# Kernel optimization log

Hardware: AMD Instinct MI355X
Metric: run time of the kernel (lower is better)

Reference implementation:

```python
import jax, jax.numpy as jnp
import numpy as np

BN, T, D_MODEL = 128, 256, 128
D_INNER, D_STATE, D_CONV, DT_RANK = 2 * D_MODEL, 16, 4, 8  # mamba-ssm defaults


def silu(v):
    return v * jax.nn.sigmoid(v)


def setup_inputs() -> dict:
    key = jax.random.key(0)
    ks = jax.random.split(key, 8)
    s = 0.02
    A_log = jnp.log(jnp.tile(jnp.arange(1, D_STATE + 1, dtype=jnp.float32), (D_INNER, 1)))
    return {
        "x": jax.random.normal(ks[0], (BN, T, D_MODEL), jnp.float32),
        "in_proj_w": jax.random.normal(ks[1], (2 * D_INNER, D_MODEL), jnp.float32) * s,
        "conv_w": jax.random.normal(ks[2], (D_INNER, 1, D_CONV), jnp.float32) * s,
        "conv_b": jnp.zeros((D_INNER,), jnp.float32),
        "x_proj_w": jax.random.normal(ks[3], (DT_RANK + 2 * D_STATE, D_INNER), jnp.float32) * s,
        "dt_proj_w": jax.random.normal(ks[4], (D_INNER, DT_RANK), jnp.float32) * s,
        "dt_proj_b": jax.random.uniform(ks[5], (D_INNER,), jnp.float32, -4.0, -2.0),
        "A_log": A_log,
        "D": jnp.ones((D_INNER,), jnp.float32),
        "out_proj_w": jax.random.normal(ks[6], (D_MODEL, D_INNER), jnp.float32) * s,
        "down_w": jax.random.normal(ks[7], (D_MODEL, D_MODEL, 3), jnp.float32) * s,
        "down_b": jnp.zeros((D_MODEL,), jnp.float32),
        "ln_g": jnp.ones((D_MODEL,), jnp.float32),
        "ln_b": jnp.zeros((D_MODEL,), jnp.float32),
    }


def _mamba(x, in_proj_w, conv_w, conv_b, x_proj_w, dt_proj_w, dt_proj_b, A_log, D, out_proj_w):
    B = x.shape[0]
    xz = jnp.einsum('bld,ed->ble', x, in_proj_w)            # (B,L,2*di)
    xc, z = jnp.split(xz, 2, axis=-1)
    # depthwise causal conv over time
    xt = xc.transpose(0, 2, 1)                               # (B,di,L)
    xt = jax.lax.conv_general_dilated(xt, conv_w, (1,), [(D_CONV - 1, 0)],
                                      feature_group_count=D_INNER)
    xc = silu((xt + conv_b[None, :, None]).transpose(0, 2, 1))  # (B,L,di)
    x_dbl = jnp.einsum('bld,ed->ble', xc, x_proj_w)
    dt, Bm, Cm = jnp.split(x_dbl, [DT_RANK, DT_RANK + D_STATE], axis=-1)
    delta = jax.nn.softplus(jnp.einsum('blr,dr->bld', dt, dt_proj_w) + dt_proj_b)  # (B,L,di)
    A = -jnp.exp(A_log)                                       # (di,N)

    def step(h, inp):
        d_t, B_t, C_t, u_t = inp                              # (B,di),(B,N),(B,N),(B,di)
        dA = jnp.exp(d_t[..., None] * A)                      # (B,di,N)
        h = dA * h + (d_t * u_t)[..., None] * B_t[:, None, :]
        return h, jnp.einsum('bdn,bn->bd', h, C_t)

    h0 = jnp.zeros((B, D_INNER, D_STATE), x.dtype)
    _, ys = jax.lax.scan(step, h0, (delta.swapaxes(0, 1), Bm.swapaxes(0, 1),
                                    Cm.swapaxes(0, 1), xc.swapaxes(0, 1)))
    y = ys.swapaxes(0, 1) + xc * D                            # (B,L,di)
    y = y * silu(z)
    return jnp.einsum('ble,de->bld', y, out_proj_w)


def reference(x, in_proj_w, conv_w, conv_b, x_proj_w, dt_proj_w, dt_proj_b,
              A_log, D, out_proj_w, down_w, down_b, ln_g, ln_b):
    x_skip = x
    h = _mamba(x, in_proj_w, conv_w, conv_b, x_proj_w, dt_proj_w, dt_proj_b,
               A_log, D, out_proj_w)                          # dropout: eval mode = identity
    ht = h.transpose(0, 2, 1)                                 # (B,d,T)
    ht = jax.lax.conv_general_dilated(ht, down_w, (2,), [(1, 1)]) + down_b[None, :, None]
    h = ht.transpose(0, 2, 1)                                 # (B,T//2,d)
    mu = jnp.mean(h, axis=-1, keepdims=True)
    var = jnp.mean((h - mu) ** 2, axis=-1, keepdims=True)
    h = (h - mu) * jax.lax.rsqrt(var + 1e-5) * ln_g + ln_b
    return (h, x_skip)
```

## Files before the change

### kernel.cpp

```cpp
#include <hip/hip_runtime.h>
#include <hip/hip_bf16.h>


typedef __attribute__((ext_vector_type(8))) short bf16x8;
typedef __attribute__((ext_vector_type(4))) short bf16x4;
typedef __attribute__((ext_vector_type(4))) float f32x4;
using bf16 = __hip_bfloat16;

static __device__ __forceinline__ short f2s(float v) {
  union { bf16 b; short s; } u; u.b = (bf16)v; return u.s;
}
static __device__ __forceinline__ float s2f(short s) {
  union { short s; bf16 b; } u; u.s = s; return (float)u.b;
}

static __device__ __forceinline__ size_t pidx(int b, int d, int t) {
  return ((((size_t)b * 8 + (d >> 5)) * 32 + (t >> 3)) * 32 + (d & 31)) * 8 + (t & 7);
}

__global__ __launch_bounds__(256) void prep_all(const float* __restrict__ x,
                                                const float* __restrict__ ipw,
                                                const float* __restrict__ xpw,
                                                const float* __restrict__ dwn,
                                                const float* __restrict__ opw,
                                                short* __restrict__ xb,
                                                float* __restrict__ out1,
                                                short* __restrict__ ipwb,
                                                short* __restrict__ wxb,
                                                short* __restrict__ G) {
  const int bid = blockIdx.x;
  if (bid < 4096) {
    int i = (bid * 256 + threadIdx.x) * 4;
    f32x4 v = *(const f32x4*)(x + i);
    bf16x4 o;
    o[0] = f2s(v[0]); o[1] = f2s(v[1]); o[2] = f2s(v[2]); o[3] = f2s(v[3]);
    *(bf16x4*)(xb + i) = o;
    *(f32x4*)(out1 + i) = v;
  } else if (bid < 4416) {
    int idx = (bid - 4096) * 256 + threadIdx.x;
    if (idx < 65536) {
      ipwb[idx] = f2s(ipw[idx]);
    } else {
      int j = idx - 65536;
      int n = j >> 8;
      wxb[j] = (n < 40) ? f2s(xpw[j]) : (short)0;
    }
  } else {
    const int jb = bid - 4416;
    const int k  = jb >> 7;
    const int co = jb & 127;
    const int e  = threadIdx.x;
    float acc = 0.f;
    for (int dm = 0; dm < 128; ++dm) {
      acc += dwn[(co * 128 + dm) * 3 + k] * opw[dm * 256 + e];
    }
    G[(size_t)(k * 128 + co) * 256 + e] = f2s(acc);
  }
}

__global__ __launch_bounds__(256, 2) void front_k(const short* __restrict__ xb,
                                                  const short* __restrict__ ipwb,
                                                  const short* __restrict__ wxb,
                                                  const float* __restrict__ cw,
                                                  const float* __restrict__ cb,
                                                  const float* __restrict__ dtw,
                                                  const float* __restrict__ dtb,
                                                  short* __restrict__ xcP,
                                                  short* __restrict__ dP,
                                                  short* __restrict__ zP,
                                                  float* __restrict__ SBC) {
  const int b  = blockIdx.x >> 2;
  const int t0 = (blockIdx.x & 3) * 64;
  const int w    = threadIdx.x >> 6;
  const int lane = threadIdx.x & 63;
  const int r16  = lane & 15;
  const int quad = lane >> 4;
  __shared__ short AL[80][136];
  __shared__ short XC[80][264];
  __shared__ short LT[64][72];
  __shared__ float DTL[64][8];
  for (int c = threadIdx.x; c < 1280; c += 256) {
    const int row = c >> 4;
    const int col = (c & 15) * 8;
    const int t = t0 - 16 + row;
    bf16x8 v = {};
    if (t >= 0) v = *(const bf16x8*)(xb + ((size_t)(b * 256 + t)) * 128 + col);
    *(bf16x8*)(&AL[row][col]) = v;
  }
  __syncthreads();
  {
    f32x4 acc[5][4] = {};
#pragma unroll
    for (int ks = 0; ks < 4; ++ks) {
      const int k0 = ks * 32;
      bf16x8 wf[4];
#pragma unroll
      for (int j = 0; j < 4; ++j)
        wf[j] = *(const bf16x8*)(ipwb +
                 (size_t)(w * 64 + j * 16 + r16) * 128 + quad * 8 + k0);
#pragma unroll
      for (int mt = 0; mt < 5; ++mt) {
        bf16x8 a = *(const bf16x8*)(&AL[mt * 16 + r16][quad * 8 + k0]);
#pragma unroll
        for (int j = 0; j < 4; ++j)
          acc[mt][j] = __builtin_amdgcn_mfma_f32_16x16x32_bf16(a, wf[j],
                                                               acc[mt][j], 0, 0, 0);
      }
    }
#pragma unroll
    for (int mt = 0; mt < 5; ++mt)
#pragma unroll
      for (int j = 0; j < 4; ++j)
#pragma unroll
        for (int r = 0; r < 4; ++r)
          XC[mt * 16 + quad * 4 + r][w * 64 + j * 16 + r16] = f2s(acc[mt][j][r]);
  }
  for (int nt = 0; nt < 4; ++nt) {
    f32x4 accz[4] = {};
#pragma unroll
    for (int ks = 0; ks < 4; ++ks) {
      const int k0 = ks * 32;
      bf16x8 a = *(const bf16x8*)(&AL[16 + w * 16 + r16][quad * 8 + k0]);
#pragma unroll
      for (int j = 0; j < 4; ++j) {
        bf16x8 wf = *(const bf16x8*)(ipwb +
                 (size_t)(256 + nt * 64 + j * 16 + r16) * 128 + quad * 8 + k0);
        accz[j] = __builtin_amdgcn_mfma_f32_16x16x32_bf16(a, wf, accz[j], 0, 0, 0);
      }
    }
    __syncthreads();
#pragma unroll
    for (int j = 0; j < 4; ++j)
#pragma unroll
      for (int r = 0; r < 4; ++r) {
        float v = accz[j][r];
        LT[j * 16 + r16][w * 16 + quad * 4 + r] = f2s(v / (1.f + __expf(-v)));
      }
    __syncthreads();
#pragma unroll
    for (int it = 0; it < 2; ++it) {
      const int dw = (threadIdx.x >> 3) + it * 32;
      const int tc = (threadIdx.x & 7) * 8;
      bf16x8 v = *(const bf16x8*)(&LT[dw][tc]);
      *(bf16x8*)(zP + pidx(b, nt * 64 + dw, t0 + tc)) = v;
    }
  }
  __syncthreads();
  bf16x8 cv[4][2];
#pragma unroll
  for (int dt_ = 0; dt_ < 4; ++dt_) {
    const int d = dt_ * 64 + lane;
    const float w0 = cw[d * 4], w1 = cw[d * 4 + 1];
    const float w2 = cw[d * 4 + 2], w3 = cw[d * 4 + 3];
    const float bias = cb[d];
    const int rb_ = 16 + w * 16;
    float p0 = s2f(XC[rb_ - 3][d]);
    float p1 = s2f(XC[rb_ - 2][d]);
    float p2 = s2f(XC[rb_ - 1][d]);
#pragma unroll
    for (int i = 0; i < 16; ++i) {
      const float cur = s2f(XC[rb_ + i][d]);
      const float a = bias + p0 * w0 + p1 * w1 + p2 * w2 + cur * w3;
      const short s = f2s(a / (1.f + __expf(-a)));
      cv[dt_][i >> 3][i & 7] = s;
      p0 = p1; p1 = p2; p2 = cur;
    }
    *(bf16x8*)(xcP + pidx(b, d, t0 + w * 16))     = cv[dt_][0];
    *(bf16x8*)(xcP + pidx(b, d, t0 + w * 16 + 8)) = cv[dt_][1];
  }
  __syncthreads();
#pragma unroll
  for (int dt_ = 0; dt_ < 4; ++dt_) {
    const int d = dt_ * 64 + lane;
#pragma unroll
    for (int i = 0; i < 16; ++i)
      XC[16 + w * 16 + i][d] = cv[dt_][i >> 3][i & 7];
  }
  __syncthreads();
  {
    f32x4 ax[4] = {};
#pragma unroll
    for (int ks = 0; ks < 8; ++ks) {
      const int k0 = ks * 32;
      bf16x8 a = *(const bf16x8*)(&XC[16 + w * 16 + r16][quad * 8 + k0]);
#pragma unroll
      for (int j = 0; j < 4; ++j) {
        bf16x8 wf = *(const bf16x8*)(wxb + (size_t)(j * 16 + r16) * 256 + quad * 8 + k0);
        ax[j] = __builtin_amdgcn_mfma_f32_16x16x32_bf16(a, wf, ax[j], 0, 0, 0);
      }
    }
#pragma unroll
    for (int j = 0; j < 4; ++j) {
      const int col = j * 16 + r16;
#pragma unroll
      for (int r = 0; r < 4; ++r) {
        const int tl = w * 16 + quad * 4 + r;
        if (col < 8) {
          DTL[tl][col] = ax[j][r];
        } else if (col < 40) {
          SBC[((size_t)b * 256 + t0 + tl) * 32 + (col - 8)] = ax[j][r];
        }
      }
    }
  }
  __syncthreads();
#pragma unroll
  for (int dt_ = 0; dt_ < 4; ++dt_) {
    const int d = dt_ * 64 + lane;
    float wd[8];
#pragma unroll
    for (int j = 0; j < 8; ++j) wd[j] = dtw[d * 8 + j];
    const float bd = dtb[d];
    bf16x8 dv0, dv1;
#pragma unroll
    for (int i = 0; i < 16; ++i) {
      const int tl = w * 16 + i;
      const f32x4 p0 = *(const f32x4*)(&DTL[tl][0]);
      const f32x4 p1 = *(const f32x4*)(&DTL[tl][4]);
      float acc = bd;
#pragma unroll
      for (int j = 0; j < 4; ++j) acc += p0[j] * wd[j] + p1[j] * wd[4 + j];
      const float delta = (acc > 20.f) ? acc : __logf(1.f + __expf(acc));
      const short s = f2s(delta);
      if (i < 8) dv0[i] = s; else dv1[i - 8] = s;
    }
    *(bf16x8*)(dP + pidx(b, d, t0 + w * 16))     = dv0;
    *(bf16x8*)(dP + pidx(b, d, t0 + w * 16 + 8)) = dv1;
  }
}

#define LDS_S(SB, CH) do {                                                   \
    _Pragma("unroll")                                                        \
    for (int j_ = 0; j_ < 8; ++j_) {                                         \
      SBr[SB][j_] = *(const f32x4*)(&S[(CH) * 8 + j_][q * 4]);               \
      SCr[SB][j_] = *(const f32x4*)(&S[(CH) * 8 + j_][16 + q * 4]);          \
    }                                                                        \
  } while (0)

#define LDG(GB, CH) do {                                                     \
    if ((CH) < 32) {                                                         \
      uu[GB] = *(const bf16x8*)(xcP + pb + (size_t)(CH) * 256);              \
      dd[GB] = *(const bf16x8*)(dP + pb + (size_t)(CH) * 256);               \
      if (q == 0) zz[GB] = *(const bf16x8*)(zP + pb + (size_t)(CH) * 256);   \
    }                                                                        \
  } while (0)

#define CHUNK(GB, SB, CH) do {                                               \
    _Pragma("unroll")                                                        \
    for (int tt_ = 0; tt_ < 8; ++tt_) {                                      \
      const int t_ = (CH) * 8 + tt_;                                         \
      const float delta_ = s2f(dd[GB][tt_]);                                 \
      const float u_ = s2f(uu[GB][tt_]);                                     \
      const float du_ = delta_ * u_;                                         \
      const f32x4 Bq_ = SBr[SB][tt_];                                        \
      const f32x4 Cq_ = SCr[SB][tt_];                                        \
      float yt_ = 0.f;                                                       \
      _Pragma("unroll")                                                      \
      for (int n_ = 0; n_ < 4; ++n_) {                                       \
        const float dA_ = __builtin_amdgcn_exp2f(delta_ * A2[n_]);           \
        h[n_] = dA_ * h[n_] + du_ * Bq_[n_];                                 \
        yt_ += h[n_] * Cq_[n_];                                              \
      }                                                                      \
      yt_ += __shfl_xor(yt_, 1);                                             \
      yt_ += __shfl_xor(yt_, 2);                                             \
      if (q == 0)                                                            \
        yb[(rb + t_) * 256 + d] = f2s((yt_ + u_ * Dv) * s2f(zz[GB][tt_]));   \
    }                                                                        \
  } while (0)

__global__ __launch_bounds__(128, 2) void scan12(const float* __restrict__ SBC,
                                                 const short* __restrict__ xcP,
                                                 const short* __restrict__ dP,
                                                 const short* __restrict__ zP,
                                                 const float* __restrict__ alog,
                                                 const float* __restrict__ Dp,
                                                 short* __restrict__ yb) {
  const int g = blockIdx.x & 7;
  const int b = blockIdx.x >> 3;
  const int q = threadIdx.x & 3;
  const int dl = threadIdx.x >> 2;
  const int d = g * 32 + dl;
  const size_t rb = (size_t)b * 256;
  __shared__ float S[256][32];
  for (int i = threadIdx.x; i < 2048; i += 128) {
    *(f32x4*)(&S[i >> 3][(i & 7) * 4]) =
        *(const f32x4*)(SBC + (size_t)b * 8192 + i * 4);
  }
  float A2[4];
#pragma unroll
  for (int n = 0; n < 4; ++n)
    A2[n] = -__expf(alog[d * 16 + q * 4 + n]) * 1.44269504089f;
  const float Dv = Dp[d];
  float h[4] = {0.f, 0.f, 0.f, 0.f};
  const size_t pb = (((size_t)b * 8 + g) * 32) * 256 + (size_t)dl * 8;
  f32x4 SBr[2][8], SCr[2][8];
  bf16x8 uu[4], dd[4];
  bf16x8 zz[4] = {};
  LDG(0, 0); LDG(1, 1); LDG(2, 2); LDG(3, 3);
  __syncthreads();
  LDS_S(0, 0);
  for (int c = 0; c < 32; c += 4) {
    LDS_S(1, c + 1);
    CHUNK(0, 0, c);
    LDG(0, c + 4);
    LDS_S(0, c + 2);
    CHUNK(1, 1, c + 1);
    LDG(1, c + 5);
    LDS_S(1, c + 3);
    CHUNK(2, 0, c + 2);
    LDG(2, c + 6);
    if (c + 4 < 32) LDS_S(0, c + 4);
    CHUNK(3, 1, c + 3);
    LDG(3, c + 7);
  }
}

__global__ __launch_bounds__(256) void od_k(const short* __restrict__ yb,
                                            const short* __restrict__ G,
                                            const float* __restrict__ db,
                                            const float* __restrict__ lng,
                                            const float* __restrict__ lnb,
                                            float* __restrict__ out) {
  const int wave = threadIdx.x >> 6;
  const int lane = threadIdx.x & 63;
  const int r16  = lane & 15;
  const int quad = lane >> 4;
  const int m_base = blockIdx.x * 64 + wave * 16;
  const int ma = m_base + r16;
  const int ba = ma >> 7, toa = ma & 127;
  f32x4 acc[8] = {};
  const bf16x8 az = {};
#pragma unroll
  for (int k = 0; k < 3; ++k) {
    const int tp = 2 * toa + k - 1;
    const bool valid = (tp >= 0) && (tp < 256);
    const int tpc = tp < 0 ? 0 : (tp > 255 ? 255 : tp);
    const short* Ap = yb + (size_t)(ba * 256 + tpc) * 256 + quad * 8;
    const short* Gp = G + (size_t)(k * 128 + r16) * 256 + quad * 8;
#pragma unroll
    for (int k0 = 0; k0 < 256; k0 += 32) {
      bf16x8 a = *(const bf16x8*)(Ap + k0);
      a = valid ? a : az;
#pragma unroll
      for (int j = 0; j < 8; ++j) {
        bf16x8 g = *(const bf16x8*)(Gp + (size_t)j * 16 * 256 + k0);
        acc[j] = __builtin_amdgcn_mfma_f32_16x16x32_bf16(a, g, acc[j], 0, 0, 0);
      }
    }
  }
  float dbv[8], g8[8], be8[8];
#pragma unroll
  for (int j = 0; j < 8; ++j) {
    const int col = j * 16 + r16;
    dbv[j] = db[col]; g8[j] = lng[col]; be8[j] = lnb[col];
  }
#pragma unroll
  for (int r = 0; r < 4; ++r) {
    float v[8];
    float s = 0.f;
#pragma unroll
    for (int j = 0; j < 8; ++j) { v[j] = acc[j][r] + dbv[j]; s += v[j]; }
    s += __shfl_xor(s, 1); s += __shfl_xor(s, 2);
    s += __shfl_xor(s, 4); s += __shfl_xor(s, 8);
    const float mu = s * (1.0f / 128.0f);
    float vs = 0.f;
#pragma unroll
    for (int j = 0; j < 8; ++j) { const float dd = v[j] - mu; vs += dd * dd; }
    vs += __shfl_xor(vs, 1); vs += __shfl_xor(vs, 2);
    vs += __shfl_xor(vs, 4); vs += __shfl_xor(vs, 8);
    const float rstd = rsqrtf(vs * (1.0f / 128.0f) + 1e-5f);
    const int rowm = m_base + quad * 4 + r;
#pragma unroll
    for (int j = 0; j < 8; ++j) {
      out[(size_t)rowm * 128 + j * 16 + r16] = (v[j] - mu) * rstd * g8[j] + be8[j];
    }
  }
}

static const size_t O_YB    = 0;
static const size_t O_XCP   = 16777216;
static const size_t O_ZP    = 33554432;
static const size_t O_DP    = 50331648;
static const size_t O_SBC   = 67108864;
static const size_t O_G     = 71303168;
static const size_t O_XB    = 75497472;
static const size_t O_IPWB  = 92274688;

extern "C" void kernel_launch(void* const* d_in, const int* in_sizes, int n_in,
                              void* d_out, int out_size, void* d_ws, size_t ws_size,
                              hipStream_t stream) {
  const float* x    = (const float*)d_in[0];
  const float* ipw  = (const float*)d_in[1];
  const float* cw   = (const float*)d_in[2];
  const float* cb   = (const float*)d_in[3];
  const float* xpw  = (const float*)d_in[4];
  const float* dtw  = (const float*)d_in[5];
  const float* dtb  = (const float*)d_in[6];
  const float* alog = (const float*)d_in[7];
  const float* Dp   = (const float*)d_in[8];
  const float* opw  = (const float*)d_in[9];
  const float* dw   = (const float*)d_in[10];
  const float* db   = (const float*)d_in[11];
  const float* lng  = (const float*)d_in[12];
  const float* lnb  = (const float*)d_in[13];

  char*  ws     = (char*)d_ws;
  short* yb     = (short*)(ws + O_YB);
  short* xcP    = (short*)(ws + O_XCP);
  short* zP     = (short*)(ws + O_ZP);
  short* dP     = (short*)(ws + O_DP);
  float* SBC    = (float*)(ws + O_SBC);
  short* G      = (short*)(ws + O_G);
  short* xb     = (short*)(ws + O_XB);
  short* ipwb   = (short*)(ws + O_IPWB);
  float* out    = (float*)d_out;
  short* wxb    = (short*)out;
  float* out1   = out + 2097152;

  prep_all<<<4800, 256, 0, stream>>>(x, ipw, xpw, dw, opw,
                                     xb, out1, ipwb, wxb, G);
  front_k<<<512, 256, 0, stream>>>(xb, ipwb, wxb, cw, cb, dtw, dtb,
                                   xcP, dP, zP, SBC);
  scan12<<<1024, 128, 0, stream>>>(SBC, xcP, dP, zP, alog, Dp, yb);
  od_k<<<256, 256, 0, stream>>>(yb, G, db, lng, lnb, out);
}
```

Measured before the change: 225.0 us.

## Fuse prep kernel into front kernel, converting fp32 inputs and weights on the fly

```diff
diff --git a/kernel.cpp b/kernel.cpp
--- a/kernel.cpp
+++ b/kernel.cpp
@@ -13,54 +13,24 @@
 static __device__ __forceinline__ float s2f(short s) {
   union { short s; bf16 b; } u; u.s = s; return (float)u.b;
 }
+static __device__ __forceinline__ bf16x8 ld8f(const float* __restrict__ p) {
+  f32x4 a = *(const f32x4*)p;
+  f32x4 b = *(const f32x4*)(p + 4);
+  bf16x8 r;
+  r[0] = f2s(a[0]); r[1] = f2s(a[1]); r[2] = f2s(a[2]); r[3] = f2s(a[3]);
+  r[4] = f2s(b[0]); r[5] = f2s(b[1]); r[6] = f2s(b[2]); r[7] = f2s(b[3]);
+  return r;
+}
 
 static __device__ __forceinline__ size_t pidx(int b, int d, int t) {
   return ((((size_t)b * 8 + (d >> 5)) * 32 + (t >> 3)) * 32 + (d & 31)) * 8 + (t & 7);
 }
 
-__global__ __launch_bounds__(256) void prep_all(const float* __restrict__ x,
-                                                const float* __restrict__ ipw,
-                                                const float* __restrict__ xpw,
-                                                const float* __restrict__ dwn,
-                                                const float* __restrict__ opw,
-                                                short* __restrict__ xb,
-                                                float* __restrict__ out1,
-                                                short* __restrict__ ipwb,
-                                                short* __restrict__ wxb,
-                                                short* __restrict__ G) {
-  const int bid = blockIdx.x;
-  if (bid < 4096) {
-    int i = (bid * 256 + threadIdx.x) * 4;
-    f32x4 v = *(const f32x4*)(x + i);
-    bf16x4 o;
-    o[0] = f2s(v[0]); o[1] = f2s(v[1]); o[2] = f2s(v[2]); o[3] = f2s(v[3]);
-    *(bf16x4*)(xb + i) = o;
-    *(f32x4*)(out1 + i) = v;
-  } else if (bid < 4416) {
-    int idx = (bid - 4096) * 256 + threadIdx.x;
-    if (idx < 65536) {
-      ipwb[idx] = f2s(ipw[idx]);
-    } else {
-      int j = idx - 65536;
-      int n = j >> 8;
-      wxb[j] = (n < 40) ? f2s(xpw[j]) : (short)0;
-    }
-  } else {
-    const int jb = bid - 4416;
-    const int k  = jb >> 7;
-    const int co = jb & 127;
-    const int e  = threadIdx.x;
-    float acc = 0.f;
-    for (int dm = 0; dm < 128; ++dm) {
-      acc += dwn[(co * 128 + dm) * 3 + k] * opw[dm * 256 + e];
-    }
-    G[(size_t)(k * 128 + co) * 256 + e] = f2s(acc);
-  }
-}
-
-__global__ __launch_bounds__(256, 2) void front_k(const short* __restrict__ xb,
-                                                  const short* __restrict__ ipwb,
-                                                  const short* __restrict__ wxb,
+__global__ __launch_bounds__(256, 2) void front_k(const float* __restrict__ x,
+                                                  const float* __restrict__ ipw,
+                                                  const float* __restrict__ xpw,
+                                                  const float* __restrict__ dwn,
+                                                  const float* __restrict__ opw,
                                                   const float* __restrict__ cw,
                                                   const float* __restrict__ cb,
                                                   const float* __restrict__ dtw,
@@ -68,7 +38,9 @@
                                                   short* __restrict__ xcP,
                                                   short* __restrict__ dP,
                                                   short* __restrict__ zP,
-                                                  float* __restrict__ SBC) {
+                                                  float* __restrict__ SBC,
+                                                  float* __restrict__ out1,
+                                                  short* __restrict__ G) {
   const int b  = blockIdx.x >> 2;
   const int t0 = (blockIdx.x & 3) * 64;
   const int w    = threadIdx.x >> 6;
@@ -79,12 +51,34 @@
   __shared__ short XC[80][264];
   __shared__ short LT[64][72];
   __shared__ float DTL[64][8];
+  if (blockIdx.x < 384) {
+    const int k  = blockIdx.x >> 7;
+    const int co = blockIdx.x & 127;
+    const int e  = threadIdx.x;
+    float acc = 0.f;
+#pragma unroll 4
+    for (int dm = 0; dm < 128; ++dm) {
+      acc += dwn[(co * 128 + dm) * 3 + k] * opw[dm * 256 + e];
+    }
+    G[(size_t)(k * 128 + co) * 256 + e] = f2s(acc);
+  }
   for (int c = threadIdx.x; c < 1280; c += 256) {
     const int row = c >> 4;
     const int col = (c & 15) * 8;
     const int t = t0 - 16 + row;
     bf16x8 v = {};
-    if (t >= 0) v = *(const bf16x8*)(xb + ((size_t)(b * 256 + t)) * 128 + col);
+    if (t >= 0) {
+      const float* src = x + ((size_t)(b * 256 + t)) * 128 + col;
+      f32x4 f0 = *(const f32x4*)src;
+      f32x4 f1 = *(const f32x4*)(src + 4);
+      v[0] = f2s(f0[0]); v[1] = f2s(f0[1]); v[2] = f2s(f0[2]); v[3] = f2s(f0[3]);
+      v[4] = f2s(f1[0]); v[5] = f2s(f1[1]); v[6] = f2s(f1[2]); v[7] = f2s(f1[3]);
+      if (row >= 16) {
+        float* dst = out1 + ((size_t)(b * 256 + t)) * 128 + col;
+        *(f32x4*)dst = f0;
+        *(f32x4*)(dst + 4) = f1;
+      }
+    }
     *(bf16x8*)(&AL[row][col]) = v;
   }
   __syncthreads();
@@ -96,8 +90,7 @@
       bf16x8 wf[4];
 #pragma unroll
       for (int j = 0; j < 4; ++j)
-        wf[j] = *(const bf16x8*)(ipwb +
-                 (size_t)(w * 64 + j * 16 + r16) * 128 + quad * 8 + k0);
+        wf[j] = ld8f(ipw + (size_t)(w * 64 + j * 16 + r16) * 128 + quad * 8 + k0);
 #pragma unroll
       for (int mt = 0; mt < 5; ++mt) {
         bf16x8 a = *(const bf16x8*)(&AL[mt * 16 + r16][quad * 8 + k0]);
@@ -123,7 +116,7 @@
       bf16x8 a = *(const bf16x8*)(&AL[16 + w * 16 + r16][quad * 8 + k0]);
 #pragma unroll
       for (int j = 0; j < 4; ++j) {
-        bf16x8 wf = *(const bf16x8*)(ipwb +
+        bf16x8 wf = ld8f(ipw +
                  (size_t)(256 + nt * 64 + j * 16 + r16) * 128 + quad * 8 + k0);
         accz[j] = __builtin_amdgcn_mfma_f32_16x16x32_bf16(a, wf, accz[j], 0, 0, 0);
       }
@@ -178,19 +171,21 @@
   }
   __syncthreads();
   {
-    f32x4 ax[4] = {};
+    f32x4 ax[3] = {};
 #pragma unroll
     for (int ks = 0; ks < 8; ++ks) {
       const int k0 = ks * 32;
       bf16x8 a = *(const bf16x8*)(&XC[16 + w * 16 + r16][quad * 8 + k0]);
 #pragma unroll
-      for (int j = 0; j < 4; ++j) {
-        bf16x8 wf = *(const bf16x8*)(wxb + (size_t)(j * 16 + r16) * 256 + quad * 8 + k0);
+      for (int j = 0; j < 3; ++j) {
+        const int wr = j * 16 + r16;
+        bf16x8 wf = {};
+        if (wr < 40) wf = ld8f(xpw + (size_t)wr * 256 + quad * 8 + k0);
         ax[j] = __builtin_amdgcn_mfma_f32_16x16x32_bf16(a, wf, ax[j], 0, 0, 0);
       }
     }
 #pragma unroll
-    for (int j = 0; j < 4; ++j) {
+    for (int j = 0; j < 3; ++j) {
       const int col = j * 16 + r16;
 #pragma unroll
       for (int r = 0; r < 4; ++r) {
@@ -383,8 +378,6 @@
 static const size_t O_DP    = 50331648;
 static const size_t O_SBC   = 67108864;
 static const size_t O_G     = 71303168;
-static const size_t O_XB    = 75497472;
-static const size_t O_IPWB  = 92274688;
 
 extern "C" void kernel_launch(void* const* d_in, const int* in_sizes, int n_in,
                               void* d_out, int out_size, void* d_ws, size_t ws_size,
@@ -411,16 +404,11 @@
   short* dP     = (short*)(ws + O_DP);
   float* SBC    = (float*)(ws + O_SBC);
   short* G      = (short*)(ws + O_G);
-  short* xb     = (short*)(ws + O_XB);
-  short* ipwb   = (short*)(ws + O_IPWB);
   float* out    = (float*)d_out;
-  short* wxb    = (short*)out;
   float* out1   = out + 2097152;
 
-  prep_all<<<4800, 256, 0, stream>>>(x, ipw, xpw, dw, opw,
-                                     xb, out1, ipwb, wxb, G);
-  front_k<<<512, 256, 0, stream>>>(xb, ipwb, wxb, cw, cb, dtw, dtb,
-                                   xcP, dP, zP, SBC);
+  front_k<<<512, 256, 0, stream>>>(x, ipw, xpw, dw, opw, cw, cb, dtw, dtb,
+                                   xcP, dP, zP, SBC, out1, G);
   scan12<<<1024, 128, 0, stream>>>(SBC, xcP, dP, zP, alog, Dp, yb);
   od_k<<<256, 256, 0, stream>>>(yb, G, db, lng, lnb, out);
 }
```

New measurement: 241.6 us. 1.07x slower.
